# Kernel optimization log

Hardware: AMD Instinct MI355X
Metric: run time of the kernel (lower is better)

Reference implementation:

```python
import jax, jax.numpy as jnp
import numpy as np

N_NODES = 100000
N_EDGES = 1600000
N_GRAPHS = 256
IN_DIM, HID = 30, 40

def setup_inputs() -> dict:
    key = jax.random.key(0)
    ks = jax.random.split(key, 12)
    x = jax.random.normal(ks[0], (N_NODES, IN_DIM), dtype=jnp.float32)
    edge_index = jax.random.randint(ks[1], (2, N_EDGES), 0, N_NODES, dtype=jnp.int64)
    batch = jnp.sort(jax.random.randint(ks[2], (N_NODES,), 0, N_GRAPHS, dtype=jnp.int64))
    def glorot(k, shape):
        lim = float(np.sqrt(6.0 / (shape[0] + shape[1])))
        return jax.random.uniform(k, shape, dtype=jnp.float32, minval=-lim, maxval=lim)
    return {
        'x': x, 'edge_index': edge_index, 'batch': batch,
        'W1': glorot(ks[3], (IN_DIM, HID)), 'b1': jnp.zeros((HID,), jnp.float32),
        'W2': glorot(ks[4], (HID, HID)),    'b2': jnp.zeros((HID,), jnp.float32),
        'W3': glorot(ks[5], (HID, HID)),    'b3': jnp.zeros((HID,), jnp.float32),
        'lin_w': glorot(ks[6], (HID, 1)),   'lin_b': jnp.zeros((1,), jnp.float32),
    }

def _gcn_layer(x, src, dst, norm, W, b, n_nodes):
    # x: [N, Fin] -> [N, Fout]; fused gather-matmul-scatter form of GCNConv
    h = x @ W                                   # dense transform first (Fout small)
    msg = h[src] * norm[:, None]                # [E+N, Fout] gather + edge scale
    out = jax.ops.segment_sum(msg, dst, num_segments=n_nodes)
    return out + b

def reference(x, edge_index, batch, W1, b1, W2, b2, W3, b3, lin_w, lin_b):
    n = x.shape[0]
    loops = jnp.arange(n, dtype=edge_index.dtype)
    src = jnp.concatenate([edge_index[0], loops])  # add self loops (GCNConv default)
    dst = jnp.concatenate([edge_index[1], loops])
    deg = jax.ops.segment_sum(jnp.ones_like(dst, dtype=x.dtype), dst, num_segments=n)
    dinv = jax.lax.rsqrt(jnp.maximum(deg, 1.0))    # deg >= 1 thanks to self loops
    norm = dinv[src] * dinv[dst]

    h = jax.nn.relu(_gcn_layer(x, src, dst, norm, W1, b1, n))  # dropout inactive (eval)
    h = jax.nn.relu(_gcn_layer(h, src, dst, norm, W2, b2, n))
    h = jax.nn.relu(_gcn_layer(h, src, dst, norm, W3, b3, n))

    # global_mean_pool over graphs
    g_sum = jax.ops.segment_sum(h, batch, num_segments=N_GRAPHS)
    cnt = jax.ops.segment_sum(jnp.ones((n,), h.dtype), batch, num_segments=N_GRAPHS)
    g = g_sum / jnp.maximum(cnt, 1.0)[:, None]
    return g @ lin_w + lin_b                      # [N_GRAPHS, 1]
```

## Files before the change

### kernel.cpp

```cpp
#include <hip/hip_runtime.h>

#define HID 40
#define RBKT 196
#define BSH 9
#define CAP 12288
#define EPB 4096


__device__ inline unsigned pack2_bf16(float a, float b) {
    unsigned ua = __float_as_uint(a);
    unsigned ub = __float_as_uint(b);
    ua = (ua + 0x7fffu + ((ua >> 16) & 1u)) >> 16;
    ub = (ub + 0x7fffu + ((ub >> 16) & 1u)) & 0xffff0000u;
    return ua | ub;
}

__device__ inline void acc8_bf16(float* acc, uint4 v) {
    acc[0] += __uint_as_float(v.x << 16);
    acc[1] += __uint_as_float(v.x & 0xffff0000u);
    acc[2] += __uint_as_float(v.y << 16);
    acc[3] += __uint_as_float(v.y & 0xffff0000u);
    acc[4] += __uint_as_float(v.z << 16);
    acc[5] += __uint_as_float(v.z & 0xffff0000u);
    acc[6] += __uint_as_float(v.w << 16);
    acc[7] += __uint_as_float(v.w & 0xffff0000u);
}

__global__ void clear_kernel(int* __restrict__ bucket_cnt, float* __restrict__ g_sum, int G) {
    int t = blockIdx.x * blockDim.x + threadIdx.x;
    if (t < RBKT) bucket_cnt[t] = 0;
    if (t < G) g_sum[t] = 0.f;
}


__global__ __launch_bounds__(256) void binA_kernel(
        const int* __restrict__ esrc, const int* __restrict__ edst, int E,
        int* __restrict__ bucket_cnt, int* __restrict__ bucket_data) {
    __shared__ int cnt_l[RBKT];
    __shared__ int base_l[RBKT];
    int t = threadIdx.x;
    for (int b = t; b < RBKT; b += 256) cnt_l[b] = 0;
    __syncthreads();
    int e0 = blockIdx.x * EPB;
    int e1 = min(e0 + EPB, E);
    for (int e = e0 + t; e < e1; e += 256) {
        atomicAdd(&cnt_l[edst[e] >> BSH], 1);
    }
    __syncthreads();
    for (int b = t; b < RBKT; b += 256) {
        int c = cnt_l[b];
        base_l[b] = (c > 0) ? atomicAdd(&bucket_cnt[b], c) : 0;
        cnt_l[b] = 0;
    }
    __syncthreads();
    for (int e = e0 + t; e < e1; e += 256) {
        int d = edst[e];
        int s = esrc[e];
        int b = d >> BSH;
        int off = base_l[b] + atomicAdd(&cnt_l[b], 1);
        if (off < CAP) bucket_data[(size_t)b * CAP + off] = (s << BSH) | (d & 511);
    }
}

__global__ void scan_buckets_kernel(const int* __restrict__ cnt, int* __restrict__ base) {
    __shared__ int s[256];
    int t = threadIdx.x;
    int c = (t < RBKT) ? min(cnt[t], CAP) : 0;
    s[t] = c;
    __syncthreads();
    for (int off = 1; off < 256; off <<= 1) {
        int y = (t >= off) ? s[t - off] : 0;
        __syncthreads();
        s[t] += y;
        __syncthreads();
    }
    if (t < RBKT) base[t] = s[t] - c;
    if (t == RBKT - 1) base[RBKT] = s[t];
}

__global__ __launch_bounds__(256) void buildB_kernel(
        const int* __restrict__ bucket_cnt, const int* __restrict__ bucket_base,
        const int* __restrict__ bucket_data,
        int* __restrict__ rowptr, int* __restrict__ mid, int* __restrict__ csr,
        float* __restrict__ dinv, int n, int half) {
    __shared__ int deg_l[512];
    __shared__ int deg_lo[512];
    __shared__ int off_lo[512];
    __shared__ int off_hi[512];
    __shared__ int ps[256];
    int r = blockIdx.x;
    int t = threadIdx.x;
    int cnt = min(bucket_cnt[r], CAP);
    int base = bucket_base[r];
    int node0 = r << BSH;
    int nr = min(512, n - node0);
    for (int i = t; i < 512; i += 256) { deg_l[i] = 0; deg_lo[i] = 0; }
    __syncthreads();
    const int* data = bucket_data + (size_t)r * CAP;
    for (int e = t; e < cnt; e += 256) {
        int v = data[e];
        atomicAdd(&deg_l[v & 511], 1);
        if ((v >> BSH) < half) atomicAdd(&deg_lo[v & 511], 1);
    }
    __syncthreads();
    int a0 = deg_l[2 * t], a1 = deg_l[2 * t + 1];
    ps[t] = a0 + a1;
    __syncthreads();
    for (int off = 1; off < 256; off <<= 1) {
        int y = (t >= off) ? ps[t - off] : 0;
        __syncthreads();
        ps[t] += y;
        __syncthreads();
    }
    int excl = ps[t] - (a0 + a1);
    off_lo[2 * t] = excl;
    off_lo[2 * t + 1] = excl + a0;
    off_hi[2 * t] = excl + deg_lo[2 * t];
    off_hi[2 * t + 1] = excl + a0 + deg_lo[2 * t + 1];
    __syncthreads();
    for (int i = t; i < nr; i += 256) {
        int rp = base + off_lo[i];
        rowptr[node0 + i] = rp;
        mid[node0 + i] = rp + deg_lo[i];
        dinv[node0 + i] = rsqrtf((float)(deg_l[i] + 1));
    }
    if (r == RBKT - 1 && t == 0) rowptr[n] = base + cnt;
    __syncthreads();
    for (int e = t; e < cnt; e += 256) {
        int v = data[e];
        int s = v >> BSH;
        int d = v & 511;
        int p = (s < half) ? atomicAdd(&off_lo[d], 1) : atomicAdd(&off_hi[d], 1);
        csr[base + p] = s;
    }
}


__global__ __launch_bounds__(256) void scale_bf16_kernel(
        const float* __restrict__ x, const float* __restrict__ dinv,
        unsigned* __restrict__ xs, int n) {
    int t = blockIdx.x * blockDim.x + threadIdx.x;
    int i = t >> 4, p = t & 15;
    if (i >= n) return;
    float a = 0.f, b = 0.f;
    if (p < 15) {
        float d = dinv[i];
        a = x[i * 30 + 2 * p] * d;
        b = x[i * 30 + 2 * p + 1] * d;
    }
    xs[(size_t)i * 16 + p] = pack2_bf16(a, b);
}

template <int TPN>
__global__ __launch_bounds__(256) void gather_bf16_kernel(
        const unsigned* __restrict__ xs, const int* __restrict__ rowptr,
        const int* __restrict__ mid, const int* __restrict__ csr,
        const float* __restrict__ dinv, unsigned* __restrict__ gout, int n) {
    int t = blockIdx.x * blockDim.x + threadIdx.x;
    int i = t / TPN;
    int q = t - i * TPN;
    if (i >= n) return;
    const uint4* tab = reinterpret_cast<const uint4*>(xs);
    float acc[8];
    {
        uint4 v = tab[(size_t)i * TPN + q];
        acc[0] = __uint_as_float(v.x << 16);
        acc[1] = __uint_as_float(v.x & 0xffff0000u);
        acc[2] = __uint_as_float(v.y << 16);
        acc[3] = __uint_as_float(v.y & 0xffff0000u);
        acc[4] = __uint_as_float(v.z << 16);
        acc[5] = __uint_as_float(v.z & 0xffff0000u);
        acc[6] = __uint_as_float(v.w << 16);
        acc[7] = __uint_as_float(v.w & 0xffff0000u);
    }
    int e0 = rowptr[i], m = mid[i], e1 = rowptr[i + 1];
    int e = e0;
    for (; e + 4 <= m; e += 4) {
        int s0 = csr[e], s1 = csr[e + 1], s2 = csr[e + 2], s3 = csr[e + 3];
        uint4 v0 = tab[(size_t)s0 * TPN + q];
        uint4 v1 = tab[(size_t)s1 * TPN + q];
        uint4 v2 = tab[(size_t)s2 * TPN + q];
        uint4 v3 = tab[(size_t)s3 * TPN + q];
        acc8_bf16(acc, v0);
        acc8_bf16(acc, v1);
        acc8_bf16(acc, v2);
        acc8_bf16(acc, v3);
    }
    for (; e < m; e++) acc8_bf16(acc, tab[(size_t)csr[e] * TPN + q]);
    for (; e + 4 <= e1; e += 4) {
        int s0 = csr[e], s1 = csr[e + 1], s2 = csr[e + 2], s3 = csr[e + 3];
        uint4 v0 = tab[(size_t)s0 * TPN + q];
        uint4 v1 = tab[(size_t)s1 * TPN + q];
        uint4 v2 = tab[(size_t)s2 * TPN + q];
        uint4 v3 = tab[(size_t)s3 * TPN + q];
        acc8_bf16(acc, v0);
        acc8_bf16(acc, v1);
        acc8_bf16(acc, v2);
        acc8_bf16(acc, v3);
    }
    for (; e < e1; e++) acc8_bf16(acc, tab[(size_t)csr[e] * TPN + q]);
    float d = dinv[i];
    uint4 o;
    o.x = pack2_bf16(acc[0] * d, acc[1] * d);
    o.y = pack2_bf16(acc[2] * d, acc[3] * d);
    o.z = pack2_bf16(acc[4] * d, acc[5] * d);
    o.w = pack2_bf16(acc[6] * d, acc[7] * d);
    reinterpret_cast<uint4*>(gout)[(size_t)i * TPN + q] = o;
}

template <int INF, int RU, bool POOL>
__global__ __launch_bounds__(256) void transform_v2_kernel(
        const unsigned* __restrict__ tin, const float* __restrict__ W,
        const float* __restrict__ bias, const float* __restrict__ dinv,
        const float* __restrict__ lin_w, const int* __restrict__ batch,
        unsigned* __restrict__ out, float* __restrict__ g_sum, int n) {
    constexpr int OUTF = 40;
    constexpr int OPF  = 20;
    __shared__ unsigned tile[256 * (RU + 1)];
    const int tid = threadIdx.x;
    const int nodeblk = blockIdx.x >> 1;
    const int slice = blockIdx.x & 1;
    const int q0 = slice * OPF;
    const int base = nodeblk * 256;
    const unsigned* g = tin + (size_t)base * RU;
    const int limit = (min(256, n - base)) * RU;
    for (int idx = tid; idx < 256 * RU; idx += 256) {
        if (idx < limit) {
            int r = idx / RU, c = idx - r * RU;
            tile[r * (RU + 1) + c] = g[idx];
        }
    }
    __syncthreads();
    const int node = base + tid;
    const bool valid = (node < n);
    float s = 0.f;
    if (valid) {
        const unsigned* myrow = &tile[tid * (RU + 1)];
        float acc[OPF];
        #pragma unroll
        for (int j = 0; j < OPF; j++) acc[j] = 0.f;
        for (int k2 = 0; k2 < INF / 2; k2++) {
            unsigned u = myrow[k2];
            float x0 = __uint_as_float(u << 16);
            float x1 = __uint_as_float(u & 0xffff0000u);
            const float* w0 = &W[(2 * k2) * OUTF + q0];
            const float* w1 = &W[(2 * k2 + 1) * OUTF + q0];
            #pragma unroll
            for (int j = 0; j < OPF; j++) acc[j] += x0 * w0[j];
            #pragma unroll
            for (int j = 0; j < OPF; j++) acc[j] += x1 * w1[j];
        }
        if (!POOL) {
            float d = dinv[node];
            unsigned* orow = out + (size_t)node * 20 + slice * 10;
            #pragma unroll
            for (int j = 0; j < OPF / 2; j++) {
                float v0 = fmaxf(acc[2 * j] + bias[q0 + 2 * j], 0.f) * d;
                float v1 = fmaxf(acc[2 * j + 1] + bias[q0 + 2 * j + 1], 0.f) * d;
                orow[j] = pack2_bf16(v0, v1);
            }
        } else {
            #pragma unroll
            for (int j = 0; j < OPF; j++) {
                s += fmaxf(acc[j] + bias[q0 + j], 0.f) * lin_w[q0 + j];
            }
        }
    }
    if (POOL) {
        int gg = batch[valid ? node : (n - 1)];
        if (!valid) s = 0.f;
        int g0 = __shfl(gg, 0, 64);
        if (__all(gg == g0)) {
            #pragma unroll
            for (int off = 32; off > 0; off >>= 1) s += __shfl_xor(s, off, 64);
            if ((tid & 63) == 0) atomicAdd(&g_sum[g0], s);
        } else {
            if (valid) atomicAdd(&g_sum[gg], s);
        }
    }
}

__global__ void finalize_kernel(const float* __restrict__ g_sum,
                                const int* __restrict__ batch,
                                const float* __restrict__ lin_b,
                                float* __restrict__ out, int n, int G) {
    int b = blockIdx.x * blockDim.x + threadIdx.x;
    if (b >= G) return;
    int lo = 0, hi = n;
    while (lo < hi) { int m = (lo + hi) >> 1; if (batch[m] < b) lo = m + 1; else hi = m; }
    int lo2 = lo, hi2 = n;
    while (lo2 < hi2) { int m = (lo2 + hi2) >> 1; if (batch[m] < b + 1) lo2 = m + 1; else hi2 = m; }
    int cnt = lo2 - lo;
    out[b] = g_sum[b] / (float)(cnt > 0 ? cnt : 1) + lin_b[0];
}


static inline size_t align_up(size_t v, size_t a) { return (v + a - 1) / a * a; }

extern "C" void kernel_launch(void* const* d_in, const int* in_sizes, int n_in,
                              void* d_out, int out_size, void* d_ws, size_t ws_size,
                              hipStream_t stream) {
    const float* x      = (const float*)d_in[0];
    const int*   esrc   = (const int*)d_in[1];
    const int*   batch  = (const int*)d_in[2];
    const float* W1     = (const float*)d_in[3];
    const float* b1     = (const float*)d_in[4];
    const float* W2     = (const float*)d_in[5];
    const float* b2     = (const float*)d_in[6];
    const float* W3     = (const float*)d_in[7];
    const float* b3     = (const float*)d_in[8];
    const float* lin_w  = (const float*)d_in[9];
    const float* lin_b  = (const float*)d_in[10];
    float* out = (float*)d_out;

    const int n = in_sizes[0] / 30;
    const int E = in_sizes[1] / 2;
    const int G = out_size;
    const int* edst = esrc + E;

    char* w = (char*)d_ws;
    size_t off = 0;
    auto take = [&](size_t bytes) { size_t o = off; off = align_up(off + bytes, 256); return (void*)(w + o); };
    int*      bucket_cnt  = (int*)take((size_t)RBKT * 4);
    int*      bucket_base = (int*)take((size_t)(RBKT + 1) * 4);
    int*      rowptr      = (int*)take((size_t)(n + 1) * 4);
    int*      mid         = (int*)take((size_t)n * 4);
    float*    dinv        = (float*)take((size_t)n * 4);
    int*      csr         = (int*)take((size_t)E * 4);
    float*    g_sum       = (float*)take((size_t)G * 4);
    size_t bd = (size_t)RBKT * CAP * 4;
    size_t x1 = (size_t)n * 16 * 4;
    void* shared_region = take(bd > x1 ? bd : x1);
    int*      bucket_data = (int*)shared_region;
    unsigned* xs1         = (unsigned*)shared_region;
    unsigned* agg         = (unsigned*)take((size_t)n * 20 * 4);
    unsigned* tbA         = (unsigned*)take((size_t)n * 20 * 4);
    unsigned* tbB         = (unsigned*)take((size_t)n * 20 * 4);
    (void)ws_size;

    clear_kernel<<<1, 256, 0, stream>>>(bucket_cnt, g_sum, G);

    binA_kernel<<<(E + EPB - 1) / EPB, 256, 0, stream>>>(esrc, edst, E, bucket_cnt, bucket_data);
    scan_buckets_kernel<<<1, 256, 0, stream>>>(bucket_cnt, bucket_base);
    buildB_kernel<<<RBKT, 256, 0, stream>>>(bucket_cnt, bucket_base, bucket_data,
                                            rowptr, mid, csr, dinv, n, n / 2);

    int nblk256 = (n + 255) / 256;

    scale_bf16_kernel<<<((size_t)n * 16 + 255) / 256, 256, 0, stream>>>(x, dinv, xs1, n);
    gather_bf16_kernel<4><<<((size_t)n * 4 + 255) / 256, 256, 0, stream>>>(
        xs1, rowptr, mid, csr, dinv, agg, n);
    transform_v2_kernel<30, 16, false><<<nblk256 * 2, 256, 0, stream>>>(
        agg, W1, b1, dinv, nullptr, nullptr, tbA, nullptr, n);
    gather_bf16_kernel<5><<<((size_t)n * 5 + 255) / 256, 256, 0, stream>>>(
        tbA, rowptr, mid, csr, dinv, agg, n);
    transform_v2_kernel<40, 20, false><<<nblk256 * 2, 256, 0, stream>>>(
        agg, W2, b2, dinv, nullptr, nullptr, tbB, nullptr, n);
    gather_bf16_kernel<5><<<((size_t)n * 5 + 255) / 256, 256, 0, stream>>>(
        tbB, rowptr, mid, csr, dinv, agg, n);
    transform_v2_kernel<40, 20, true><<<nblk256 * 2, 256, 0, stream>>>(
        agg, W3, b3, dinv, lin_w, batch, nullptr, g_sum, n);

    finalize_kernel<<<1, 256, 0, stream>>>(g_sum, batch, lin_b, out, n, G);
}
```

Measured before the change: 244.9 us.

## Replace scalar FMA node transforms with bf16 MFMA 16x16x32 tiles

Rewrites the three per-layer dense transform kernels to use MFMA bf16 matrix instructions. Each wave handles 16 nodes and computes three 16-column output tiles, with weights packed to bf16 in registers. The change removes the LDS tile staging and the split into two column slices, and pooling now reduces through a small shared array. In exchange, weights are rounded to bf16, the output tile is padded to 48 columns, and outputs are written with strided 4-byte stores after a shuffle.

```diff
diff --git a/kernel.cpp b/kernel.cpp
--- a/kernel.cpp
+++ b/kernel.cpp
@@ -6,6 +6,11 @@
 #define CAP 12288
 #define EPB 4096
 
+
+typedef __attribute__((ext_vector_type(4))) unsigned uv4;
+typedef __attribute__((ext_vector_type(8))) __bf16 bf16x8;
+typedef __attribute__((ext_vector_type(8))) unsigned short usv8;
+typedef __attribute__((ext_vector_type(4))) float f32x4;
 
 __device__ inline unsigned pack2_bf16(float a, float b) {
     unsigned ua = __float_as_uint(a);
@@ -208,74 +213,113 @@
     reinterpret_cast<uint4*>(gout)[(size_t)i * TPN + q] = o;
 }
 
-template <int INF, int RU, bool POOL>
-__global__ __launch_bounds__(256) void transform_v2_kernel(
+template <int INF, int RQ, bool POOL>
+__global__ __launch_bounds__(256) void transform_mfma_kernel(
         const unsigned* __restrict__ tin, const float* __restrict__ W,
         const float* __restrict__ bias, const float* __restrict__ dinv,
         const float* __restrict__ lin_w, const int* __restrict__ batch,
         unsigned* __restrict__ out, float* __restrict__ g_sum, int n) {
-    constexpr int OUTF = 40;
-    constexpr int OPF  = 20;
-    __shared__ unsigned tile[256 * (RU + 1)];
+    constexpr int KST = (INF > 32) ? 2 : 1;
+    __shared__ float sarr[64];
     const int tid = threadIdx.x;
-    const int nodeblk = blockIdx.x >> 1;
-    const int slice = blockIdx.x & 1;
-    const int q0 = slice * OPF;
-    const int base = nodeblk * 256;
-    const unsigned* g = tin + (size_t)base * RU;
-    const int limit = (min(256, n - base)) * RU;
-    for (int idx = tid; idx < 256 * RU; idx += 256) {
-        if (idx < limit) {
-            int r = idx / RU, c = idx - r * RU;
-            tile[r * (RU + 1) + c] = g[idx];
-        }
-    }
-    __syncthreads();
-    const int node = base + tid;
-    const bool valid = (node < n);
-    float s = 0.f;
-    if (valid) {
-        const unsigned* myrow = &tile[tid * (RU + 1)];
-        float acc[OPF];
+    const int wv = tid >> 6;
+    const int l = tid & 63;
+    const int lr = l & 15;
+    const int lg = l >> 4;
+    usv8 wf[KST][3];
+    #pragma unroll
+    for (int kst = 0; kst < KST; kst++) {
         #pragma unroll
-        for (int j = 0; j < OPF; j++) acc[j] = 0.f;
-        for (int k2 = 0; k2 < INF / 2; k2++) {
-            unsigned u = myrow[k2];
-            float x0 = __uint_as_float(u << 16);
-            float x1 = __uint_as_float(u & 0xffff0000u);
-            const float* w0 = &W[(2 * k2) * OUTF + q0];
-            const float* w1 = &W[(2 * k2 + 1) * OUTF + q0];
+        for (int ct = 0; ct < 3; ct++) {
             #pragma unroll
-            for (int j = 0; j < OPF; j++) acc[j] += x0 * w0[j];
+            for (int i = 0; i < 8; i++) {
+                int kb = kst * 32 + lg * 8 + i;
+                int col = ct * 16 + lr;
+                float f = (kb < INF && col < 40) ? W[kb * 40 + col] : 0.f;
+                wf[kst][ct][i] = (unsigned short)(pack2_bf16(f, 0.f) & 0xffffu);
+            }
+        }
+    }
+    const int node0 = blockIdx.x * 64 + wv * 16;
+    const uv4* tab = reinterpret_cast<const uv4*>(tin);
+    const int arow = node0 + lr;
+    uv4 zq = {0u, 0u, 0u, 0u};
+    uv4 a0q = (arow < n) ? tab[(size_t)arow * RQ + lg] : zq;
+    bf16x8 a0 = __builtin_bit_cast(bf16x8, a0q);
+    bf16x8 a1;
+    if constexpr (KST == 2) {
+        uv4 a1q = (arow < n && lg == 0) ? tab[(size_t)arow * RQ + 4] : zq;
+        a1 = __builtin_bit_cast(bf16x8, a1q);
+    }
+    f32x4 acc[3];
+    #pragma unroll
+    for (int ct = 0; ct < 3; ct++) {
+        f32x4 z = {0.f, 0.f, 0.f, 0.f};
+        acc[ct] = __builtin_amdgcn_mfma_f32_16x16x32_bf16(
+            a0, __builtin_bit_cast(bf16x8, wf[0][ct]), z, 0, 0, 0);
+        if constexpr (KST == 2) {
+            acc[ct] = __builtin_amdgcn_mfma_f32_16x16x32_bf16(
+                a1, __builtin_bit_cast(bf16x8, wf[1][ct]), acc[ct], 0, 0, 0);
+        }
+    }
+    int noder[4]; float dr[4]; bool vr[4];
+    #pragma unroll
+    for (int r = 0; r < 4; r++) {
+        noder[r] = node0 + lg * 4 + r;
+        vr[r] = (noder[r] < n);
+        dr[r] = vr[r] ? dinv[noder[r]] : 0.f;
+    }
+    if (!POOL) {
+        #pragma unroll
+        for (int ct = 0; ct < 3; ct++) {
+            int col = ct * 16 + lr;
+            float bc = (col < 40) ? bias[col] : 0.f;
             #pragma unroll
-            for (int j = 0; j < OPF; j++) acc[j] += x1 * w1[j];
-        }
-        if (!POOL) {
-            float d = dinv[node];
-            unsigned* orow = out + (size_t)node * 20 + slice * 10;
+            for (int r = 0; r < 4; r++) {
+                float v = fmaxf(acc[ct][r] + bc, 0.f) * dr[r];
+                float pv = __shfl_xor(v, 1, 64);
+                if (((lr & 1) == 0) && vr[r] && col < 40) {
+                    out[(size_t)noder[r] * 20 + ct * 8 + (lr >> 1)] = pack2_bf16(v, pv);
+                }
+            }
+        }
+    } else {
+        float s[4] = {0.f, 0.f, 0.f, 0.f};
+        #pragma unroll
+        for (int ct = 0; ct < 3; ct++) {
+            int col = ct * 16 + lr;
+            float bc = (col < 40) ? bias[col] : 0.f;
+            float lwv = (col < 40) ? lin_w[col] : 0.f;
             #pragma unroll
-            for (int j = 0; j < OPF / 2; j++) {
-                float v0 = fmaxf(acc[2 * j] + bias[q0 + 2 * j], 0.f) * d;
-                float v1 = fmaxf(acc[2 * j + 1] + bias[q0 + 2 * j + 1], 0.f) * d;
-                orow[j] = pack2_bf16(v0, v1);
+            for (int r = 0; r < 4; r++)
+                s[r] += fmaxf(acc[ct][r] + bc, 0.f) * lwv;
+        }
+        #pragma unroll
+        for (int r = 0; r < 4; r++) if (!vr[r]) s[r] = 0.f;
+        #pragma unroll
+        for (int mask = 1; mask <= 8; mask <<= 1) {
+            #pragma unroll
+            for (int r = 0; r < 4; r++) s[r] += __shfl_xor(s[r], mask, 64);
+        }
+        if (lr == 0) {
+            #pragma unroll
+            for (int r = 0; r < 4; r++) sarr[wv * 16 + lg * 4 + r] = s[r];
+        }
+        __syncthreads();
+        if (tid < 64) {
+            float ss = sarr[tid];
+            int node2 = blockIdx.x * 64 + tid;
+            bool v2 = (node2 < n);
+            int gg = batch[v2 ? node2 : (n - 1)];
+            if (!v2) ss = 0.f;
+            int g0 = __shfl(gg, 0, 64);
+            if (__all(gg == g0)) {
+                #pragma unroll
+                for (int off2 = 32; off2 > 0; off2 >>= 1) ss += __shfl_xor(ss, off2, 64);
+                if (tid == 0) atomicAdd(&g_sum[g0], ss);
+            } else {
+                if (v2) atomicAdd(&g_sum[gg], ss);
             }
-        } else {
-            #pragma unroll
-            for (int j = 0; j < OPF; j++) {
-                s += fmaxf(acc[j] + bias[q0 + j], 0.f) * lin_w[q0 + j];
-            }
-        }
-    }
-    if (POOL) {
-        int gg = batch[valid ? node : (n - 1)];
-        if (!valid) s = 0.f;
-        int g0 = __shfl(gg, 0, 64);
-        if (__all(gg == g0)) {
-            #pragma unroll
-            for (int off = 32; off > 0; off >>= 1) s += __shfl_xor(s, off, 64);
-            if ((tid & 63) == 0) atomicAdd(&g_sum[g0], s);
-        } else {
-            if (valid) atomicAdd(&g_sum[gg], s);
         }
     }
 }
@@ -345,20 +389,20 @@
     buildB_kernel<<<RBKT, 256, 0, stream>>>(bucket_cnt, bucket_base, bucket_data,
                                             rowptr, mid, csr, dinv, n, n / 2);
 
-    int nblk256 = (n + 255) / 256;
+    int nblkT = (n + 63) / 64;
 
     scale_bf16_kernel<<<((size_t)n * 16 + 255) / 256, 256, 0, stream>>>(x, dinv, xs1, n);
     gather_bf16_kernel<4><<<((size_t)n * 4 + 255) / 256, 256, 0, stream>>>(
         xs1, rowptr, mid, csr, dinv, agg, n);
-    transform_v2_kernel<30, 16, false><<<nblk256 * 2, 256, 0, stream>>>(
+    transform_mfma_kernel<30, 4, false><<<nblkT, 256, 0, stream>>>(
         agg, W1, b1, dinv, nullptr, nullptr, tbA, nullptr, n);
     gather_bf16_kernel<5><<<((size_t)n * 5 + 255) / 256, 256, 0, stream>>>(
         tbA, rowptr, mid, csr, dinv, agg, n);
-    transform_v2_kernel<40, 20, false><<<nblk256 * 2, 256, 0, stream>>>(
+    transform_mfma_kernel<40, 5, false><<<nblkT, 256, 0, stream>>>(
         agg, W2, b2, dinv, nullptr, nullptr, tbB, nullptr, n);
     gather_bf16_kernel<5><<<((size_t)n * 5 + 255) / 256, 256, 0, stream>>>(
         tbB, rowptr, mid, csr, dinv, agg, n);
-    transform_v2_kernel<40, 20, true><<<nblk256 * 2, 256, 0, stream>>>(
+    transform_mfma_kernel<40, 5, true><<<nblkT, 256, 0, stream>>>(
         agg, W3, b3, dinv, lin_w, batch, nullptr, g_sum, n);
 
     finalize_kernel<<<1, 256, 0, stream>>>(g_sum, batch, lin_b, out, n, G);
```

New measurement: 205.3 us. 16.2% less time.
